# Performance work log

Hardware: AMD Instinct MI355X
Metric: run time of the kernel (lower is better)

## Reference

```python
import jax, jax.numpy as jnp
import numpy as np

B, H, S, D = 512, 1024, 1024, 128
TOPK = 32

def setup_inputs() -> dict:
    key = jax.random.key(0)
    ks = jax.random.split(key, 12)
    w = lambda k, shape: (jax.random.normal(k, shape, dtype=jnp.float32) * 0.02)
    return {
        "latent": jax.random.normal(ks[0], (B, H), dtype=jnp.float32),
        "memory": jax.random.normal(ks[1], (B, S, D), dtype=jnp.float32),
        "read_query_w": w(ks[2], (H, D)),
        "read_query_b": jnp.zeros((D,), jnp.float32),
        "memory_key": w(ks[3], (S, D)),
        "write_gate_w": w(ks[4], (H + D, 1)),
        "write_gate_b": jnp.zeros((1,), jnp.float32),
        "dmd_proj_w": w(ks[5], (H + D, 1)),
        "dmd_proj_b": jnp.zeros((1,), jnp.float32),
        "phase_proj_w": w(ks[6], (H, 1)),
        "phase_proj_b": jnp.zeros((1,), jnp.float32),
        "write_value_w": w(ks[7], (H, D)),
        "write_value_b": jnp.zeros((D,), jnp.float32),
    }

def reference(latent, memory, read_query_w, read_query_b, memory_key,
              write_gate_w, write_gate_b, dmd_proj_w, dmd_proj_b,
              phase_proj_w, phase_proj_b, write_value_w, write_value_b):
    # soft read over memory slots
    query = latent @ read_query_w + read_query_b              # [B, D]
    logits = jnp.einsum('bd,sd->bs', query, memory_key)       # [B, S]
    weights = jax.nn.softmax(logits, axis=-1)
    # top-k masked renormalization (topk=32 < S)
    _, topk_idx = jax.lax.top_k(weights, TOPK)                # [B, K]
    rows = jnp.arange(weights.shape[0])[:, None]
    mask = jnp.zeros_like(weights).at[rows, topk_idx].set(1.0)
    weights = weights * mask
    weights = weights / jnp.clip(weights.sum(-1, keepdims=True), 1e-8)
    read = jnp.einsum('bs,bsd->bd', weights, memory)          # [B, D]
    gate_input = jnp.concatenate([latent, read], axis=-1)     # [B, H+D]
    # sigmoid gate (gating_mode='sigmoid')
    gate = jax.nn.sigmoid(gate_input @ write_gate_w + write_gate_b)  # [B, 1]
    # dmd gating
    dmd_signal = jnp.tanh(gate_input @ dmd_proj_w + dmd_proj_b)
    gate = jnp.clip(gate * (0.75 + 0.5 * (dmd_signal + 1.0) * 0.5), 0.0, 1.0)
    # phase gating
    phase = latent @ phase_proj_w + phase_proj_b
    gate = gate * (0.5 * (1.0 + jnp.cos(phase)))
    # soft scatter-write update
    value = (latent @ write_value_w + write_value_b)[:, None, :]      # [B, 1, D]
    gw = gate[:, :, None] * weights[:, :, None]                       # [B, S, 1]
    new_memory = (1.0 - gw) * memory + gw * value                     # [B, S, D]
    return read, new_memory, weights
```

## Files before the change

kernel.cpp:

```cpp
#include <hip/hip_runtime.h>
#include <math.h>

#define NB 512
#define NH 1024
#define NS 1024
#define ND 128
#define NK 32

__global__ __launch_bounds__(256) void compute_kernel(
    const float* __restrict__ latent,
    const float* __restrict__ memory,
    const float* __restrict__ rq_w,
    const float* __restrict__ rq_b,
    const float* __restrict__ mem_key,
    const float* __restrict__ wg_w,
    const float* __restrict__ wg_b,
    const float* __restrict__ dmd_w,
    const float* __restrict__ dmd_b,
    const float* __restrict__ ph_w,
    const float* __restrict__ ph_b,
    const float* __restrict__ wv_w,
    const float* __restrict__ wv_b,
    float* __restrict__ out_read,
    float* __restrict__ out_wts,
    float* __restrict__ gates,
    float* __restrict__ valw)
{
  const int b   = blockIdx.x;
  const int tid = threadIdx.x;

  __shared__ float lat[NH];
  __shared__ float lg[NS];
  __shared__ float qv[ND];
  __shared__ float part[256];
  __shared__ float rd[ND];
  __shared__ float tv[NK];
  __shared__ int   ti[NK];
  __shared__ float wk[NK];
  __shared__ float redv[4];
  __shared__ int   redi[4];
  __shared__ float scal[4];

  for (int h = tid; h < NH; h += 256) lat[h] = latent[(size_t)b * NH + h];
  __syncthreads();

  {
    const int d = tid & 127, p = tid >> 7;
    float acc = 0.f;
    const float* W = rq_w + (size_t)p * 512 * ND + d;
    const float* L = lat + p * 512;
    #pragma unroll 8
    for (int h = 0; h < 512; ++h) acc += L[h] * W[(size_t)h * ND];
    part[tid] = acc;
  }
  __syncthreads();
  if (tid < ND) qv[tid] = part[tid] + part[tid + 128] + rq_b[tid];
  __syncthreads();

  {
    const float4* q4 = (const float4*)qv;
    for (int j = 0; j < 4; ++j) {
      int s = tid + j * 256;
      const float4* k4 = (const float4*)(mem_key + (size_t)s * ND);
      float acc = 0.f;
      #pragma unroll
      for (int i = 0; i < ND / 4; ++i) {
        float4 kv = k4[i]; float4 qq = q4[i];
        acc += kv.x * qq.x + kv.y * qq.y + kv.z * qq.z + kv.w * qq.w;
      }
      lg[s] = acc;
    }
  }
  __syncthreads();

  const float NEGINF = -3.0e38f;
  for (int kk = 0; kk < NK; ++kk) {
    float best = NEGINF; int bi = 0;
    #pragma unroll
    for (int j = 0; j < 4; ++j) {
      int s = tid + j * 256;
      float v = lg[s];
      if (v > best) { best = v; bi = s; }
    }
    #pragma unroll
    for (int off = 32; off > 0; off >>= 1) {
      float ov = __shfl_down(best, off);
      int   oi = __shfl_down(bi,   off);
      if (ov > best) { best = ov; bi = oi; }
    }
    if ((tid & 63) == 0) { redv[tid >> 6] = best; redi[tid >> 6] = bi; }
    __syncthreads();
    if (tid == 0) {
      float bv = redv[0]; int bb = redi[0];
      #pragma unroll
      for (int w = 1; w < 4; ++w) if (redv[w] > bv) { bv = redv[w]; bb = redi[w]; }
      tv[kk] = bv; ti[kk] = bb; lg[bb] = NEGINF;
    }
    __syncthreads();
  }

  if (tid < 64) {
    float e = (tid < NK) ? expf(tv[tid] - tv[0]) : 0.f;
    if (tid < NK) wk[tid] = e;
    float s = e;
    #pragma unroll
    for (int off = 32; off > 0; off >>= 1) s += __shfl_down(s, off);
    if (tid == 0) scal[0] = s;
  }
  __syncthreads();
  if (tid < NK) wk[tid] = wk[tid] / scal[0];
  __syncthreads();

  if (tid < ND) {
    float r = 0.f;
    const float* mb = memory + (size_t)b * NS * ND;
    #pragma unroll 4
    for (int k = 0; k < NK; ++k) r += wk[k] * mb[(size_t)ti[k] * ND + tid];
    rd[tid] = r;
    out_read[(size_t)b * ND + tid] = r;
  }
  __syncthreads();

  {
    float p1 = 0.f, p2 = 0.f, p3 = 0.f;
    for (int h = tid; h < NH; h += 256) {
      float l = lat[h];
      p1 += l * wg_w[h]; p2 += l * dmd_w[h]; p3 += l * ph_w[h];
    }
    if (tid < ND) {
      float r = rd[tid];
      p1 += r * wg_w[NH + tid]; p2 += r * dmd_w[NH + tid];
    }
    #pragma unroll
    for (int off = 32; off > 0; off >>= 1) {
      p1 += __shfl_down(p1, off);
      p2 += __shfl_down(p2, off);
      p3 += __shfl_down(p3, off);
    }
    if ((tid & 63) == 0) { int w = tid >> 6; redv[w] = p1; part[w] = p2; part[8 + w] = p3; }
    __syncthreads();
    if (tid == 0) {
      float z1 = redv[0] + redv[1] + redv[2] + redv[3] + wg_b[0];
      float z2 = part[0] + part[1] + part[2] + part[3] + dmd_b[0];
      float z3 = part[8] + part[9] + part[10] + part[11] + ph_b[0];
      float g  = 1.f / (1.f + expf(-z1));
      float dm = tanhf(z2);
      g = g * (0.75f + 0.25f * (dm + 1.f));
      g = fminf(fmaxf(g, 0.f), 1.f);
      g = g * (0.5f * (1.f + cosf(z3)));
      scal[1] = g;
      gates[b] = g;
    }
    __syncthreads();
  }

  {
    const int d = tid & 127, p = tid >> 7;
    float acc = 0.f;
    const float* W = wv_w + (size_t)p * 512 * ND + d;
    const float* L = lat + p * 512;
    #pragma unroll 8
    for (int h = 0; h < 512; ++h) acc += L[h] * W[(size_t)h * ND];
    part[tid] = acc;
  }
  __syncthreads();
  if (tid < ND) valw[(size_t)b * ND + tid] = part[tid] + part[tid + 128] + wv_b[tid];

  for (int j = 0; j < 4; ++j) {
    int s = tid + j * 256;
    float w = 0.f;
    #pragma unroll
    for (int t = 0; t < NK; ++t) if (ti[t] == s) w = wk[t];
    out_wts[(size_t)b * NS + s] = w;
  }
}

__global__ __launch_bounds__(256) void copy_blend_kernel(
    const float* __restrict__ memory,
    const float* __restrict__ wts,
    const float* __restrict__ gates,
    const float* __restrict__ valw,
    float* __restrict__ out_mem)
{
  const long long total4 = (long long)NB * NS * ND / 4;
  const long long stride = (long long)gridDim.x * blockDim.x;
  for (long long i = (long long)blockIdx.x * blockDim.x + threadIdx.x;
       i < total4; i += stride) {
    long long e = i << 2;
    int row = (int)(e >> 7);
    float4 m = ((const float4*)memory)[i];
    float4 o = m;
    float w = wts[row];
    if (w != 0.f) {
      int b  = row >> 10;
      float g = gates[b] * w;
      const float4 v = *(const float4*)(valw + ((size_t)b << 7) + (e & 127));
      o.x = m.x + g * (v.x - m.x);
      o.y = m.y + g * (v.y - m.y);
      o.z = m.z + g * (v.z - m.z);
      o.w = m.w + g * (v.w - m.w);
    }
    ((float4*)out_mem)[i] = o;
  }
}

extern "C" void kernel_launch(void* const* d_in, const int* in_sizes, int n_in,
                              void* d_out, int out_size, void* d_ws, size_t ws_size,
                              hipStream_t stream) {
  const float* latent  = (const float*)d_in[0];
  const float* memory  = (const float*)d_in[1];
  const float* rq_w    = (const float*)d_in[2];
  const float* rq_b    = (const float*)d_in[3];
  const float* mem_key = (const float*)d_in[4];
  const float* wg_w    = (const float*)d_in[5];
  const float* wg_b    = (const float*)d_in[6];
  const float* dmd_w   = (const float*)d_in[7];
  const float* dmd_b   = (const float*)d_in[8];
  const float* ph_w    = (const float*)d_in[9];
  const float* ph_b    = (const float*)d_in[10];
  const float* wv_w    = (const float*)d_in[11];
  const float* wv_b    = (const float*)d_in[12];

  float* out_read = (float*)d_out;
  float* out_mem  = out_read + (size_t)NB * ND;
  float* out_wts  = out_mem + (size_t)NB * NS * ND;

  float* gates = (float*)d_ws;
  float* valw  = gates + 512;

  compute_kernel<<<NB, 256, 0, stream>>>(
      latent, memory, rq_w, rq_b, mem_key, wg_w, wg_b, dmd_w, dmd_b,
      ph_w, ph_b, wv_w, wv_b, out_read, out_wts, gates, valw);

  copy_blend_kernel<<<8192, 256, 0, stream>>>(memory, out_wts, gates, valw, out_mem);
}
```

Measured before the change: 590.9 us.

## Use 512-thread compute blocks with warp-local top-k and nontemporal blend

The compute kernel now runs 512 threads per batch row. Top-k becomes a two-stage selection: each wavefront picks its own 32 candidates with register shuffles, then one wavefront merges the 256 candidates, replacing 32 block-wide barrier rounds. Gate times weight is precomputed per slot into a workspace array. The blend kernel uses a fixed 8-iteration unrolled loop with nontemporal loads and stores. This adds a 2 MB workspace write and ties the grid math to the fixed problem size.

New measurement: 548.1 us. 1.08x faster.

```diff
diff --git a/kernel.cpp b/kernel.cpp
--- a/kernel.cpp
+++ b/kernel.cpp
@@ -7,7 +7,9 @@
 #define ND 128
 #define NK 32
 
-__global__ __launch_bounds__(256) void compute_kernel(
+typedef float fx4 __attribute__((ext_vector_type(4)));
+
+__global__ __launch_bounds__(512) void compute_kernel(
     const float* __restrict__ latent,
     const float* __restrict__ memory,
     const float* __restrict__ rq_w,
@@ -23,184 +25,205 @@
     const float* __restrict__ wv_b,
     float* __restrict__ out_read,
     float* __restrict__ out_wts,
-    float* __restrict__ gates,
+    float* __restrict__ gw_out,
     float* __restrict__ valw)
 {
-  const int b   = blockIdx.x;
-  const int tid = threadIdx.x;
+  const int b    = blockIdx.x;
+  const int tid  = threadIdx.x;
+  const int lane = tid & 63;
+  const int wv   = tid >> 6;
 
   __shared__ float lat[NH];
-  __shared__ float lg[NS];
+  __shared__ float wfull[NS];
+  __shared__ float part[512];
   __shared__ float qv[ND];
-  __shared__ float part[256];
   __shared__ float rd[ND];
-  __shared__ float tv[NK];
-  __shared__ int   ti[NK];
-  __shared__ float wk[NK];
-  __shared__ float redv[4];
-  __shared__ int   redi[4];
-  __shared__ float scal[4];
-
-  for (int h = tid; h < NH; h += 256) lat[h] = latent[(size_t)b * NH + h];
+  __shared__ float tvw[256];
+  __shared__ int   tiw[256];
+  __shared__ float wkL[NK];
+  __shared__ int   tiL[NK];
+  __shared__ float gred[24];
+  __shared__ float scal[2];
+
+  lat[tid]       = latent[(size_t)b * NH + tid];
+  lat[tid + 512] = latent[(size_t)b * NH + tid + 512];
   __syncthreads();
 
   {
     const int d = tid & 127, p = tid >> 7;
+    const float* W = rq_w + (size_t)(p * 256) * ND + d;
+    const float* L = lat + p * 256;
     float acc = 0.f;
-    const float* W = rq_w + (size_t)p * 512 * ND + d;
-    const float* L = lat + p * 512;
     #pragma unroll 8
-    for (int h = 0; h < 512; ++h) acc += L[h] * W[(size_t)h * ND];
+    for (int h = 0; h < 256; ++h) acc = fmaf(L[h], W[(size_t)h * ND], acc);
     part[tid] = acc;
   }
   __syncthreads();
-  if (tid < ND) qv[tid] = part[tid] + part[tid + 128] + rq_b[tid];
-  __syncthreads();
-
+  if (tid < ND)
+    qv[tid] = part[tid] + part[tid + 128] + part[tid + 256] + part[tid + 384] + rq_b[tid];
+  __syncthreads();
+
+  float r0 = 0.f, r1 = 0.f;
   {
     const float4* q4 = (const float4*)qv;
-    for (int j = 0; j < 4; ++j) {
-      int s = tid + j * 256;
-      const float4* k4 = (const float4*)(mem_key + (size_t)s * ND);
-      float acc = 0.f;
+    const float4* k0 = (const float4*)(mem_key + (size_t)tid * ND);
+    const float4* k1 = (const float4*)(mem_key + (size_t)(tid + 512) * ND);
+    #pragma unroll 8
+    for (int i = 0; i < ND / 4; ++i) {
+      float4 q = q4[i];
+      float4 x = k0[i];
+      float4 y = k1[i];
+      r0 += q.x * x.x + q.y * x.y + q.z * x.z + q.w * x.w;
+      r1 += q.x * y.x + q.y * y.y + q.z * y.z + q.w * y.w;
+    }
+  }
+
+  const float NEGINF = -3.0e38f;
+  {
+    const int s0 = tid, s1 = tid + 512;
+    float v0 = r0, v1 = r1;
+    for (int kk = 0; kk < NK; ++kk) {
+      float best; int bi;
+      if (v0 >= v1) { best = v0; bi = s0; } else { best = v1; bi = s1; }
       #pragma unroll
-      for (int i = 0; i < ND / 4; ++i) {
-        float4 kv = k4[i]; float4 qq = q4[i];
-        acc += kv.x * qq.x + kv.y * qq.y + kv.z * qq.z + kv.w * qq.w;
+      for (int off = 1; off < 64; off <<= 1) {
+        float ov = __shfl_xor(best, off);
+        int   oi = __shfl_xor(bi, off);
+        if (ov > best || (ov == best && oi < bi)) { best = ov; bi = oi; }
       }
-      lg[s] = acc;
-    }
-  }
-  __syncthreads();
-
-  const float NEGINF = -3.0e38f;
-  for (int kk = 0; kk < NK; ++kk) {
-    float best = NEGINF; int bi = 0;
-    #pragma unroll
-    for (int j = 0; j < 4; ++j) {
-      int s = tid + j * 256;
-      float v = lg[s];
-      if (v > best) { best = v; bi = s; }
-    }
-    #pragma unroll
-    for (int off = 32; off > 0; off >>= 1) {
-      float ov = __shfl_down(best, off);
-      int   oi = __shfl_down(bi,   off);
-      if (ov > best) { best = ov; bi = oi; }
-    }
-    if ((tid & 63) == 0) { redv[tid >> 6] = best; redi[tid >> 6] = bi; }
-    __syncthreads();
-    if (tid == 0) {
-      float bv = redv[0]; int bb = redi[0];
+      if (lane == 0) { tvw[(wv << 5) + kk] = best; tiw[(wv << 5) + kk] = bi; }
+      if (bi == s0) v0 = NEGINF;
+      if (bi == s1) v1 = NEGINF;
+    }
+  }
+  wfull[tid] = 0.f; wfull[tid + 512] = 0.f;
+  __syncthreads();
+
+  float selv = NEGINF; int seli = -1; float wkreg = 0.f;
+  if (wv == 0) {
+    float m0 = tvw[lane], m1 = tvw[lane + 64], m2 = tvw[lane + 128], m3 = tvw[lane + 192];
+    int   i0 = tiw[lane], i1 = tiw[lane + 64], i2 = tiw[lane + 128], i3 = tiw[lane + 192];
+    for (int kk = 0; kk < NK; ++kk) {
+      float best = m0; int bi = i0;
+      if (m1 > best || (m1 == best && i1 < bi)) { best = m1; bi = i1; }
+      if (m2 > best || (m2 == best && i2 < bi)) { best = m2; bi = i2; }
+      if (m3 > best || (m3 == best && i3 < bi)) { best = m3; bi = i3; }
       #pragma unroll
-      for (int w = 1; w < 4; ++w) if (redv[w] > bv) { bv = redv[w]; bb = redi[w]; }
-      tv[kk] = bv; ti[kk] = bb; lg[bb] = NEGINF;
-    }
-    __syncthreads();
-  }
-
-  if (tid < 64) {
-    float e = (tid < NK) ? expf(tv[tid] - tv[0]) : 0.f;
-    if (tid < NK) wk[tid] = e;
+      for (int off = 1; off < 64; off <<= 1) {
+        float ov = __shfl_xor(best, off);
+        int   oi = __shfl_xor(bi, off);
+        if (ov > best || (ov == best && oi < bi)) { best = ov; bi = oi; }
+      }
+      if (kk == lane) { selv = best; seli = bi; }
+      if (bi == i0) m0 = NEGINF;
+      if (bi == i1) m1 = NEGINF;
+      if (bi == i2) m2 = NEGINF;
+      if (bi == i3) m3 = NEGINF;
+    }
+    float maxv = __shfl(selv, 0);
+    float e = (lane < NK) ? expf(selv - maxv) : 0.f;
     float s = e;
     #pragma unroll
-    for (int off = 32; off > 0; off >>= 1) s += __shfl_down(s, off);
-    if (tid == 0) scal[0] = s;
-  }
-  __syncthreads();
-  if (tid < NK) wk[tid] = wk[tid] / scal[0];
-  __syncthreads();
-
+    for (int off = 1; off < 64; off <<= 1) s += __shfl_xor(s, off);
+    wkreg = e / s;
+    if (lane < NK) { wkL[lane] = wkreg; tiL[lane] = seli; }
+  }
+  __syncthreads();
+
+  if (wv == 0 && lane < NK) wfull[seli] = wkreg;
+  {
+    const int d = tid & 127, p = tid >> 7;
+    const float* mb = memory + (size_t)b * NS * ND;
+    float racc = 0.f;
+    #pragma unroll
+    for (int k = p * 8; k < p * 8 + 8; ++k)
+      racc = fmaf(wkL[k], mb[(size_t)tiL[k] * ND + d], racc);
+    part[tid] = racc;
+  }
+  __syncthreads();
   if (tid < ND) {
-    float r = 0.f;
-    const float* mb = memory + (size_t)b * NS * ND;
-    #pragma unroll 4
-    for (int k = 0; k < NK; ++k) r += wk[k] * mb[(size_t)ti[k] * ND + tid];
+    float r = part[tid] + part[tid + 128] + part[tid + 256] + part[tid + 384];
     rd[tid] = r;
     out_read[(size_t)b * ND + tid] = r;
   }
   __syncthreads();
 
   {
-    float p1 = 0.f, p2 = 0.f, p3 = 0.f;
-    for (int h = tid; h < NH; h += 256) {
-      float l = lat[h];
-      p1 += l * wg_w[h]; p2 += l * dmd_w[h]; p3 += l * ph_w[h];
-    }
+    float l0 = lat[tid], l1 = lat[tid + 512];
+    float p1 = l0 * wg_w[tid]  + l1 * wg_w[tid + 512];
+    float p2 = l0 * dmd_w[tid] + l1 * dmd_w[tid + 512];
+    float p3 = l0 * ph_w[tid]  + l1 * ph_w[tid + 512];
     if (tid < ND) {
       float r = rd[tid];
-      p1 += r * wg_w[NH + tid]; p2 += r * dmd_w[NH + tid];
-    }
-    #pragma unroll
-    for (int off = 32; off > 0; off >>= 1) {
-      p1 += __shfl_down(p1, off);
-      p2 += __shfl_down(p2, off);
-      p3 += __shfl_down(p3, off);
-    }
-    if ((tid & 63) == 0) { int w = tid >> 6; redv[w] = p1; part[w] = p2; part[8 + w] = p3; }
-    __syncthreads();
-    if (tid == 0) {
-      float z1 = redv[0] + redv[1] + redv[2] + redv[3] + wg_b[0];
-      float z2 = part[0] + part[1] + part[2] + part[3] + dmd_b[0];
-      float z3 = part[8] + part[9] + part[10] + part[11] + ph_b[0];
-      float g  = 1.f / (1.f + expf(-z1));
-      float dm = tanhf(z2);
-      g = g * (0.75f + 0.25f * (dm + 1.f));
-      g = fminf(fmaxf(g, 0.f), 1.f);
-      g = g * (0.5f * (1.f + cosf(z3)));
-      scal[1] = g;
-      gates[b] = g;
-    }
-    __syncthreads();
-  }
-
+      p1 += r * wg_w[NH + tid];
+      p2 += r * dmd_w[NH + tid];
+    }
+    #pragma unroll
+    for (int off = 1; off < 64; off <<= 1) {
+      p1 += __shfl_xor(p1, off);
+      p2 += __shfl_xor(p2, off);
+      p3 += __shfl_xor(p3, off);
+    }
+    if (lane == 0) { gred[wv] = p1; gred[8 + wv] = p2; gred[16 + wv] = p3; }
+  }
   {
     const int d = tid & 127, p = tid >> 7;
+    const float* W = wv_w + (size_t)(p * 256) * ND + d;
+    const float* L = lat + p * 256;
     float acc = 0.f;
-    const float* W = wv_w + (size_t)p * 512 * ND + d;
-    const float* L = lat + p * 512;
     #pragma unroll 8
-    for (int h = 0; h < 512; ++h) acc += L[h] * W[(size_t)h * ND];
+    for (int h = 0; h < 256; ++h) acc = fmaf(L[h], W[(size_t)h * ND], acc);
     part[tid] = acc;
   }
   __syncthreads();
-  if (tid < ND) valw[(size_t)b * ND + tid] = part[tid] + part[tid + 128] + wv_b[tid];
-
-  for (int j = 0; j < 4; ++j) {
-    int s = tid + j * 256;
-    float w = 0.f;
-    #pragma unroll
-    for (int t = 0; t < NK; ++t) if (ti[t] == s) w = wk[t];
-    out_wts[(size_t)b * NS + s] = w;
+
+  if (tid == 0) {
+    float z1 = wg_b[0], z2 = dmd_b[0], z3 = ph_b[0];
+    #pragma unroll
+    for (int k = 0; k < 8; ++k) { z1 += gred[k]; z2 += gred[8 + k]; z3 += gred[16 + k]; }
+    float g  = 1.f / (1.f + expf(-z1));
+    float dm = tanhf(z2);
+    g = g * (0.75f + 0.25f * (dm + 1.f));
+    g = fminf(fmaxf(g, 0.f), 1.f);
+    g = g * (0.5f * (1.f + cosf(z3)));
+    scal[0] = g;
+  }
+  __syncthreads();
+
+  {
+    const float g = scal[0];
+    float w0 = wfull[tid], w1 = wfull[tid + 512];
+    out_wts[(size_t)b * NS + tid]       = w0;
+    out_wts[(size_t)b * NS + tid + 512] = w1;
+    gw_out [(size_t)b * NS + tid]       = g * w0;
+    gw_out [(size_t)b * NS + tid + 512] = g * w1;
+    if (tid < ND)
+      valw[(size_t)b * ND + tid] =
+          part[tid] + part[tid + 128] + part[tid + 256] + part[tid + 384] + wv_b[tid];
   }
 }
 
 __global__ __launch_bounds__(256) void copy_blend_kernel(
     const float* __restrict__ memory,
-    const float* __restrict__ wts,
-    const float* __restrict__ gates,
+    const float* __restrict__ gw,
     const float* __restrict__ valw,
     float* __restrict__ out_mem)
 {
-  const long long total4 = (long long)NB * NS * ND / 4;
-  const long long stride = (long long)gridDim.x * blockDim.x;
-  for (long long i = (long long)blockIdx.x * blockDim.x + threadIdx.x;
-       i < total4; i += stride) {
-    long long e = i << 2;
-    int row = (int)(e >> 7);
-    float4 m = ((const float4*)memory)[i];
-    float4 o = m;
-    float w = wts[row];
-    if (w != 0.f) {
-      int b  = row >> 10;
-      float g = gates[b] * w;
-      const float4 v = *(const float4*)(valw + ((size_t)b << 7) + (e & 127));
-      o.x = m.x + g * (v.x - m.x);
-      o.y = m.y + g * (v.y - m.y);
-      o.z = m.z + g * (v.z - m.z);
-      o.w = m.w + g * (v.w - m.w);
-    }
-    ((float4*)out_mem)[i] = o;
+  const size_t t = (size_t)blockIdx.x * 256 + threadIdx.x;
+  const size_t stride = (size_t)8192 * 256;
+  #pragma unroll
+  for (int j = 0; j < 8; ++j) {
+    size_t i = t + (size_t)j * stride;
+    fx4 m = __builtin_nontemporal_load((const fx4*)memory + i);
+    int row = (int)(i >> 5);
+    float wgt = gw[row];
+    fx4 o = m;
+    if (wgt != 0.f) {
+      float omw = 1.f - wgt;
+      const fx4 v = *((const fx4*)valw + (size_t)((row >> 10) << 5) + (i & 31));
+      o = omw * m + wgt * v;
+    }
+    __builtin_nontemporal_store(o, (fx4*)out_mem + i);
   }
 }
 
@@ -225,12 +248,12 @@
   float* out_mem  = out_read + (size_t)NB * ND;
   float* out_wts  = out_mem + (size_t)NB * NS * ND;
 
-  float* gates = (float*)d_ws;
-  float* valw  = gates + 512;
-
-  compute_kernel<<<NB, 256, 0, stream>>>(
+  float* gw   = (float*)d_ws;
+  float* valw = gw + (size_t)NB * NS;
+
+  compute_kernel<<<NB, 512, 0, stream>>>(
       latent, memory, rq_w, rq_b, mem_key, wg_w, wg_b, dmd_w, dmd_b,
-      ph_w, ph_b, wv_w, wv_b, out_read, out_wts, gates, valw);
-
-  copy_blend_kernel<<<8192, 256, 0, stream>>>(memory, out_wts, gates, valw, out_mem);
+      ph_w, ph_b, wv_w, wv_b, out_read, out_wts, gw, valw);
+
+  copy_blend_kernel<<<8192, 256, 0, stream>>>(memory, gw, valw, out_mem);
 }
```
